# Optimization experiments

Measured on AMD Instinct MI355X. Metric: run time of the kernel, lower is better.

The kernel has to match this reference:

```python
import jax, jax.numpy as jnp
import numpy as np


def hadamard_matrix(n):
    # Sylvester construction; n must be a power of 2.
    H = np.array([[1.0]], dtype=np.float32)
    while H.shape[0] < n:
        H = np.block([[H, H], [H, -H]])
    return H


def setup_inputs() -> dict:
    key = jax.random.key(0)
    k1, k2, k3 = jax.random.split(key, 3)
    B, C, Hh, Ww, P = 8, 64, 256, 256, 4
    x = jax.random.normal(k1, (B, C, Hh, Ww), dtype=jnp.float32)
    v = jax.random.uniform(k2, (P, Hh, Ww), dtype=jnp.float32)          # torch.rand init
    T = jax.random.uniform(k3, (P, Hh, Ww), dtype=jnp.float32) / 10.0   # torch.rand/10 init
    return {"x": x, "v": v, "T": T}


def _wht2d(u, Hm, sc):
    # normalized Walsh-Hadamard transform along last two axes (H symmetric)
    u = jnp.einsum('...hw,vw->...hv', u, Hm) * sc   # axis=-1
    u = jnp.einsum('...hv,gh->...gv', u, Hm) * sc   # axis=-2
    return u


def reference(x, v, T):
    n = x.shape[-1]  # 256, power of 2; height_pad==height so no padding
    Hm = jnp.asarray(hadamard_matrix(n), dtype=x.dtype)
    sc = jnp.asarray(1.0 / np.sqrt(n), dtype=x.dtype)
    f2 = _wht2d(x, Hm, sc)                              # (B,C,H,W)
    a = f2[None] * v[:, None, None]                     # (P,B,C,H,W)
    st = jnp.tanh(a) * jax.nn.relu(jnp.abs(a) - jnp.abs(T)[:, None, None])
    f6 = st.sum(axis=0)                                 # (B,C,H,W)
    f8 = _wht2d(f6, Hm, sc)
    return f8 + x                                       # residual=True
```

## Files before the change

kernel.cpp:

```cpp
#include <hip/hip_runtime.h>
#include <hip/hip_fp16.h>


#define NROWS (8 * 64 * 256)
#define NPX   65536

__device__ __forceinline__ unsigned int h2u(__half2 h) {
  union { __half2 h; unsigned int u; } c; c.h = h; return c.u;
}
__device__ __forceinline__ __half2 u2h(unsigned int u) {
  union { __half2 h; unsigned int u; } c; c.u = u; return c.h;
}

__device__ __forceinline__ void fwht16(float f[16]) {
  #pragma unroll
  for (int d = 1; d < 16; d <<= 1) {
    #pragma unroll
    for (int i = 0; i < 16; ++i) {
      if (!(i & d)) {
        float a = f[i], b = f[i | d];
        f[i]     = a + b;
        f[i | d] = a - b;
      }
    }
  }
}

__device__ __forceinline__ void fwht256_wave(float r[4], int lane) {
  float a0 = r[0] + r[1], b0 = r[0] - r[1];
  float a1 = r[2] + r[3], b1 = r[2] - r[3];
  r[0] = a0 + a1; r[1] = b0 + b1; r[2] = a0 - a1; r[3] = b0 - b1;
  #pragma unroll
  for (int m = 1; m <= 32; m <<= 1) {
    const float s = (lane & m) ? -1.0f : 1.0f;
    #pragma unroll
    for (int j = 0; j < 4; ++j) {
      float t = __shfl_xor(r[j], m);
      r[j] = fmaf(r[j], s, t);
    }
  }
}

__device__ __forceinline__ float g_term(float a, float absT) {
  float ax = fabsf(a);
  float rl = fmaxf(ax - absT, 0.0f);
  float e  = __builtin_amdgcn_exp2f(ax * 2.8853900817779268f);
  float th = 1.0f - 2.0f * __builtin_amdgcn_rcpf(e + 1.0f);
  return copysignf(th, a) * rl;
}

__global__ __launch_bounds__(256) void k_row_fwd(const float* __restrict__ x,
                                                 __half* __restrict__ t1) {
  const int lane = threadIdx.x & 63;
  const int wave = blockIdx.x * (blockDim.x >> 6) + (threadIdx.x >> 6);
  const int nw   = gridDim.x * (blockDim.x >> 6);
  for (int row = wave; row < NROWS; row += nw) {
    const float4 xv = *reinterpret_cast<const float4*>(x + (size_t)row * 256 + lane * 4);
    float r[4] = {xv.x, xv.y, xv.z, xv.w};
    fwht256_wave(r, lane);
    const float SC = 0.0625f;
    uint2 pk;
    pk.x = h2u(__floats2half2_rn(r[0] * SC, r[1] * SC));
    pk.y = h2u(__floats2half2_rn(r[2] * SC, r[3] * SC));
    *reinterpret_cast<uint2*>(t1 + (size_t)row * 256 + lane * 4) = pk;
  }
}

__global__ __launch_bounds__(256) void k_col(const __half* t1, __half* t2,
                                             const float* __restrict__ v,
                                             const float* __restrict__ T) {
  __shared__ __align__(16) __half lds[256][72];
  const int tid = threadIdx.x;
  const int q   = tid & 15;
  const int g   = tid >> 4;
  const int img = blockIdx.x >> 2;
  const int w0  = (blockIdx.x & 3) * 64;
  const int wq  = w0 + 4 * q;
  const size_t ibase = (size_t)img * NPX;
  const float SC = 0.0625f;

  float f[4][16];

  #pragma unroll
  for (int k = 0; k < 16; ++k) {
    const int h = 16 * g + k;
    uint2 d = *reinterpret_cast<const uint2*>(t1 + ibase + (size_t)h * 256 + wq);
    float2 lo = __half22float2(u2h(d.x));
    float2 hi = __half22float2(u2h(d.y));
    f[0][k] = lo.x; f[1][k] = lo.y; f[2][k] = hi.x; f[3][k] = hi.y;
  }
  #pragma unroll
  for (int c = 0; c < 4; ++c) fwht16(f[c]);
  #pragma unroll
  for (int k = 0; k < 16; ++k) {
    const int h = 16 * g + k;
    uint2 d;
    d.x = h2u(__floats2half2_rn(f[0][k], f[1][k]));
    d.y = h2u(__floats2half2_rn(f[2][k], f[3][k]));
    *reinterpret_cast<uint2*>(&lds[h][4 * q]) = d;
  }
  __syncthreads();

  #pragma unroll
  for (int a = 0; a < 16; ++a) {
    const int h = g + 16 * a;
    uint2 d = *reinterpret_cast<uint2*>(&lds[h][4 * q]);
    float2 lo = __half22float2(u2h(d.x));
    float2 hi = __half22float2(u2h(d.y));
    f[0][a] = lo.x; f[1][a] = lo.y; f[2][a] = hi.x; f[3][a] = hi.y;
  }
  #pragma unroll
  for (int c = 0; c < 4; ++c) fwht16(f[c]);
  #pragma unroll
  for (int c = 0; c < 4; ++c)
    #pragma unroll
    for (int a = 0; a < 16; ++a) f[c][a] *= SC;

  #pragma unroll
  for (int a = 0; a < 16; ++a) {
    const int h = g + 16 * a;
    const size_t off = (size_t)h * 256 + wq;
    float acc0 = 0.f, acc1 = 0.f, acc2 = 0.f, acc3 = 0.f;
    #pragma unroll
    for (int p = 0; p < 4; ++p) {
      const float4 vv = *reinterpret_cast<const float4*>(v + (size_t)p * NPX + off);
      const float4 tt = *reinterpret_cast<const float4*>(T + (size_t)p * NPX + off);
      acc0 += g_term(f[0][a] * vv.x, fabsf(tt.x));
      acc1 += g_term(f[1][a] * vv.y, fabsf(tt.y));
      acc2 += g_term(f[2][a] * vv.z, fabsf(tt.z));
      acc3 += g_term(f[3][a] * vv.w, fabsf(tt.w));
    }
    f[0][a] = acc0; f[1][a] = acc1; f[2][a] = acc2; f[3][a] = acc3;
  }
  #pragma unroll
  for (int c = 0; c < 4; ++c) fwht16(f[c]);
  #pragma unroll
  for (int c = 0; c < 4; ++c)
    #pragma unroll
    for (int a = 0; a < 16; ++a) f[c][a] *= SC;

  #pragma unroll
  for (int a = 0; a < 16; ++a) {
    const int h = g + 16 * a;
    uint2 d;
    d.x = h2u(__floats2half2_rn(f[0][a], f[1][a]));
    d.y = h2u(__floats2half2_rn(f[2][a], f[3][a]));
    *reinterpret_cast<uint2*>(&lds[h][4 * q]) = d;
  }
  __syncthreads();

  #pragma unroll
  for (int k = 0; k < 16; ++k) {
    const int h = 16 * g + k;
    uint2 d = *reinterpret_cast<uint2*>(&lds[h][4 * q]);
    float2 lo = __half22float2(u2h(d.x));
    float2 hi = __half22float2(u2h(d.y));
    f[0][k] = lo.x; f[1][k] = lo.y; f[2][k] = hi.x; f[3][k] = hi.y;
  }
  #pragma unroll
  for (int c = 0; c < 4; ++c) fwht16(f[c]);
  #pragma unroll
  for (int k = 0; k < 16; ++k) {
    const int h = 16 * g + k;
    uint2 d;
    d.x = h2u(__floats2half2_rn(f[0][k], f[1][k]));
    d.y = h2u(__floats2half2_rn(f[2][k], f[3][k]));
    *reinterpret_cast<uint2*>(t2 + ibase + (size_t)h * 256 + wq) = d;
  }
}

__global__ __launch_bounds__(256) void k_row_bwd(const __half* __restrict__ t2,
                                                 const float* __restrict__ x,
                                                 float* __restrict__ out) {
  const int lane = threadIdx.x & 63;
  const int wave = blockIdx.x * (blockDim.x >> 6) + (threadIdx.x >> 6);
  const int nw   = gridDim.x * (blockDim.x >> 6);
  for (int row = wave; row < NROWS; row += nw) {
    uint2 pk = *reinterpret_cast<const uint2*>(t2 + (size_t)row * 256 + lane * 4);
    float2 lo = __half22float2(u2h(pk.x));
    float2 hi = __half22float2(u2h(pk.y));
    float r[4] = {lo.x, lo.y, hi.x, hi.y};
    fwht256_wave(r, lane);
    const float4 xv = *reinterpret_cast<const float4*>(x + (size_t)row * 256 + lane * 4);
    const float SC = 0.0625f;
    float4 o;
    o.x = fmaf(r[0], SC, xv.x);
    o.y = fmaf(r[1], SC, xv.y);
    o.z = fmaf(r[2], SC, xv.z);
    o.w = fmaf(r[3], SC, xv.w);
    *reinterpret_cast<float4*>(out + (size_t)row * 256 + lane * 4) = o;
  }
}

extern "C" void kernel_launch(void* const* d_in, const int* in_sizes, int n_in,
                              void* d_out, int out_size, void* d_ws, size_t ws_size,
                              hipStream_t stream) {
  const float* x = (const float*)d_in[0];
  const float* v = (const float*)d_in[1];
  const float* T = (const float*)d_in[2];
  float* out = (float*)d_out;
  __half* t1 = (__half*)d_ws;

  k_row_fwd<<<2048, 256, 0, stream>>>(x, t1);
  k_col<<<2048, 256, 0, stream>>>(t1, t1, v, T);
  k_row_bwd<<<2048, 256, 0, stream>>>(t1, x, out);
}
```

Measured before the change: 182.5 us.

## Fuse row and column Hadamard passes into one per-image kernel using LDS

Replaces the three-kernel pipeline with one kernel per image (512 blocks of 1024 threads). It holds the whole 256x256 fp16 image in 128KB of dynamic LDS, so the fp16 intermediates never go through global memory. This removes the workspace write/read traffic and two launches. In exchange, only one block fits per CU, at about 16 waves, with 64 float registers per thread under a 1024-thread launch bound. The unpadded LDS layout with stride 256 halves may also cause bank conflicts on the column accesses.

```diff
diff --git a/kernel.cpp b/kernel.cpp
--- a/kernel.cpp
+++ b/kernel.cpp
@@ -2,8 +2,8 @@
 #include <hip/hip_fp16.h>
 
 
-#define NROWS (8 * 64 * 256)
-#define NPX   65536
+#define NPX 65536
+#define SC  0.0625f
 
 __device__ __forceinline__ unsigned int h2u(__half2 h) {
   union { __half2 h; unsigned int u; } c; c.h = h; return c.u;
@@ -49,42 +49,35 @@
   return copysignf(th, a) * rl;
 }
 
-__global__ __launch_bounds__(256) void k_row_fwd(const float* __restrict__ x,
-                                                 __half* __restrict__ t1) {
-  const int lane = threadIdx.x & 63;
-  const int wave = blockIdx.x * (blockDim.x >> 6) + (threadIdx.x >> 6);
-  const int nw   = gridDim.x * (blockDim.x >> 6);
-  for (int row = wave; row < NROWS; row += nw) {
-    const float4 xv = *reinterpret_cast<const float4*>(x + (size_t)row * 256 + lane * 4);
+__global__ __launch_bounds__(1024) void k_fused(const float* __restrict__ x,
+                                                const float* __restrict__ v,
+                                                const float* __restrict__ T,
+                                                float* __restrict__ out) {
+  extern __shared__ __half S[];
+  const int tid  = threadIdx.x;
+  const int lane = tid & 63;
+  const int wv   = tid >> 6;
+  const size_t pbase = (size_t)blockIdx.x * NPX;
+
+  for (int rr = 0; rr < 16; ++rr) {
+    const int row = wv * 16 + rr;
+    const float4 xv = *reinterpret_cast<const float4*>(x + pbase + (size_t)row * 256 + 4 * lane);
     float r[4] = {xv.x, xv.y, xv.z, xv.w};
     fwht256_wave(r, lane);
-    const float SC = 0.0625f;
     uint2 pk;
     pk.x = h2u(__floats2half2_rn(r[0] * SC, r[1] * SC));
     pk.y = h2u(__floats2half2_rn(r[2] * SC, r[3] * SC));
-    *reinterpret_cast<uint2*>(t1 + (size_t)row * 256 + lane * 4) = pk;
+    *reinterpret_cast<uint2*>(&S[row * 256 + 4 * lane]) = pk;
   }
-}
+  __syncthreads();
 
-__global__ __launch_bounds__(256) void k_col(const __half* t1, __half* t2,
-                                             const float* __restrict__ v,
-                                             const float* __restrict__ T) {
-  __shared__ __align__(16) __half lds[256][72];
-  const int tid = threadIdx.x;
-  const int q   = tid & 15;
-  const int g   = tid >> 4;
-  const int img = blockIdx.x >> 2;
-  const int w0  = (blockIdx.x & 3) * 64;
-  const int wq  = w0 + 4 * q;
-  const size_t ibase = (size_t)img * NPX;
-  const float SC = 0.0625f;
-
+  const int q = tid & 63;
+  const int g = tid >> 6;
   float f[4][16];
 
   #pragma unroll
   for (int k = 0; k < 16; ++k) {
-    const int h = 16 * g + k;
-    uint2 d = *reinterpret_cast<const uint2*>(t1 + ibase + (size_t)h * 256 + wq);
+    uint2 d = *reinterpret_cast<uint2*>(&S[(16 * g + k) * 256 + 4 * q]);
     float2 lo = __half22float2(u2h(d.x));
     float2 hi = __half22float2(u2h(d.y));
     f[0][k] = lo.x; f[1][k] = lo.y; f[2][k] = hi.x; f[3][k] = hi.y;
@@ -93,18 +86,16 @@
   for (int c = 0; c < 4; ++c) fwht16(f[c]);
   #pragma unroll
   for (int k = 0; k < 16; ++k) {
-    const int h = 16 * g + k;
     uint2 d;
     d.x = h2u(__floats2half2_rn(f[0][k], f[1][k]));
     d.y = h2u(__floats2half2_rn(f[2][k], f[3][k]));
-    *reinterpret_cast<uint2*>(&lds[h][4 * q]) = d;
+    *reinterpret_cast<uint2*>(&S[(16 * g + k) * 256 + 4 * q]) = d;
   }
   __syncthreads();
 
   #pragma unroll
   for (int a = 0; a < 16; ++a) {
-    const int h = g + 16 * a;
-    uint2 d = *reinterpret_cast<uint2*>(&lds[h][4 * q]);
+    uint2 d = *reinterpret_cast<uint2*>(&S[(g + 16 * a) * 256 + 4 * q]);
     float2 lo = __half22float2(u2h(d.x));
     float2 hi = __half22float2(u2h(d.y));
     f[0][a] = lo.x; f[1][a] = lo.y; f[2][a] = hi.x; f[3][a] = hi.y;
@@ -118,8 +109,7 @@
 
   #pragma unroll
   for (int a = 0; a < 16; ++a) {
-    const int h = g + 16 * a;
-    const size_t off = (size_t)h * 256 + wq;
+    const size_t off = (size_t)(g + 16 * a) * 256 + 4 * q;
     float acc0 = 0.f, acc1 = 0.f, acc2 = 0.f, acc3 = 0.f;
     #pragma unroll
     for (int p = 0; p < 4; ++p) {
@@ -138,21 +128,18 @@
   for (int c = 0; c < 4; ++c)
     #pragma unroll
     for (int a = 0; a < 16; ++a) f[c][a] *= SC;
-
   #pragma unroll
   for (int a = 0; a < 16; ++a) {
-    const int h = g + 16 * a;
     uint2 d;
     d.x = h2u(__floats2half2_rn(f[0][a], f[1][a]));
     d.y = h2u(__floats2half2_rn(f[2][a], f[3][a]));
-    *reinterpret_cast<uint2*>(&lds[h][4 * q]) = d;
+    *reinterpret_cast<uint2*>(&S[(g + 16 * a) * 256 + 4 * q]) = d;
   }
   __syncthreads();
 
   #pragma unroll
   for (int k = 0; k < 16; ++k) {
-    const int h = 16 * g + k;
-    uint2 d = *reinterpret_cast<uint2*>(&lds[h][4 * q]);
+    uint2 d = *reinterpret_cast<uint2*>(&S[(16 * g + k) * 256 + 4 * q]);
     float2 lo = __half22float2(u2h(d.x));
     float2 hi = __half22float2(u2h(d.y));
     f[0][k] = lo.x; f[1][k] = lo.y; f[2][k] = hi.x; f[3][k] = hi.y;
@@ -161,34 +148,27 @@
   for (int c = 0; c < 4; ++c) fwht16(f[c]);
   #pragma unroll
   for (int k = 0; k < 16; ++k) {
-    const int h = 16 * g + k;
     uint2 d;
     d.x = h2u(__floats2half2_rn(f[0][k], f[1][k]));
     d.y = h2u(__floats2half2_rn(f[2][k], f[3][k]));
-    *reinterpret_cast<uint2*>(t2 + ibase + (size_t)h * 256 + wq) = d;
+    *reinterpret_cast<uint2*>(&S[(16 * g + k) * 256 + 4 * q]) = d;
   }
-}
+  __syncthreads();
 
-__global__ __launch_bounds__(256) void k_row_bwd(const __half* __restrict__ t2,
-                                                 const float* __restrict__ x,
-                                                 float* __restrict__ out) {
-  const int lane = threadIdx.x & 63;
-  const int wave = blockIdx.x * (blockDim.x >> 6) + (threadIdx.x >> 6);
-  const int nw   = gridDim.x * (blockDim.x >> 6);
-  for (int row = wave; row < NROWS; row += nw) {
-    uint2 pk = *reinterpret_cast<const uint2*>(t2 + (size_t)row * 256 + lane * 4);
+  for (int rr = 0; rr < 16; ++rr) {
+    const int row = wv * 16 + rr;
+    uint2 pk = *reinterpret_cast<uint2*>(&S[row * 256 + 4 * lane]);
     float2 lo = __half22float2(u2h(pk.x));
     float2 hi = __half22float2(u2h(pk.y));
     float r[4] = {lo.x, lo.y, hi.x, hi.y};
     fwht256_wave(r, lane);
-    const float4 xv = *reinterpret_cast<const float4*>(x + (size_t)row * 256 + lane * 4);
-    const float SC = 0.0625f;
+    const float4 xv = *reinterpret_cast<const float4*>(x + pbase + (size_t)row * 256 + 4 * lane);
     float4 o;
     o.x = fmaf(r[0], SC, xv.x);
     o.y = fmaf(r[1], SC, xv.y);
     o.z = fmaf(r[2], SC, xv.z);
     o.w = fmaf(r[3], SC, xv.w);
-    *reinterpret_cast<float4*>(out + (size_t)row * 256 + lane * 4) = o;
+    *reinterpret_cast<float4*>(out + pbase + (size_t)row * 256 + 4 * lane) = o;
   }
 }
 
@@ -199,9 +179,9 @@
   const float* v = (const float*)d_in[1];
   const float* T = (const float*)d_in[2];
   float* out = (float*)d_out;
-  __half* t1 = (__half*)d_ws;
 
-  k_row_fwd<<<2048, 256, 0, stream>>>(x, t1);
-  k_col<<<2048, 256, 0, stream>>>(t1, t1, v, T);
-  k_row_bwd<<<2048, 256, 0, stream>>>(t1, x, out);
+  const int lds_bytes = 256 * 256 * (int)sizeof(__half);
+  (void)hipFuncSetAttribute(reinterpret_cast<const void*>(k_fused),
+                            hipFuncAttributeMaxDynamicSharedMemorySize, lds_bytes);
+  k_fused<<<512, 1024, lds_bytes, stream>>>(x, v, T, out);
 }
```

Measured after the change: 327.2 us. +79.3%, slower.
